# Kernel optimization log

Measured on AMD Instinct MI355X. Metric: run time of the kernel, lower is better.

## Reference

```python
import jax, jax.numpy as jnp
import numpy as np

NUM_TYPES = 8
IN_FEATURES = 1024
OUT_FEATURES = 1024
N = 65536


def setup_inputs() -> dict:
    key = jax.random.key(0)
    k_x, k_t, k_w, k_b = jax.random.split(key, 4)
    x = jax.random.normal(k_x, (N, IN_FEATURES), dtype=jnp.float32)
    types = jnp.sort(jax.random.randint(k_t, (N,), 0, NUM_TYPES, dtype=jnp.int32))
    # Per-type Linear params; PyTorch Linear stores weight as [out, in] and
    # computes x @ W.T + b. We store W as [T, in, out] (pre-transposed).
    bound = 1.0 / np.sqrt(IN_FEATURES)
    W = jax.random.uniform(k_w, (NUM_TYPES, IN_FEATURES, OUT_FEATURES), dtype=jnp.float32,
                           minval=-bound, maxval=bound)
    b = jax.random.uniform(k_b, (NUM_TYPES, OUT_FEATURES), dtype=jnp.float32,
                           minval=-bound, maxval=bound)
    return {"x": x, "types": types, "W": W, "b": b}


def reference(x, types, W, b):
    # out[n] = x[n] @ W[types[n]] + b[types[n]]
    # Small fixed loop over num_types: one masked GEMM per type (grouped GEMM).
    num_types = W.shape[0]
    out = jnp.zeros((x.shape[0], W.shape[2]), dtype=x.dtype)
    for t in range(num_types):
        mask = (types == t)[:, None]  # [N, 1]
        out = out + jnp.where(mask, x @ W[t] + b[t], 0.0)
    return out
```

## Files before the change

kernel.cpp:

```cpp
#include <hip/hip_runtime.h>
#include <hip/hip_bf16.h>

#define NROWS 65536
#define KDIM  1024
#define NOUT  1024
#define NTYPE 8

typedef __attribute__((ext_vector_type(8))) short bf16x8;
typedef __attribute__((ext_vector_type(4))) float f32x4;

__device__ __forceinline__ unsigned int pk2_rn(float a, float b) {
  unsigned int ua = __float_as_uint(a);
  unsigned int ub = __float_as_uint(b);
  ua += 0x7fffu + ((ua >> 16) & 1u);
  ub += 0x7fffu + ((ub >> 16) & 1u);
  return (ua >> 16) | (ub & 0xffff0000u);
}

__device__ __forceinline__ void async_cp16(const void* g, void* l) {
  __builtin_amdgcn_global_load_lds(
      (const __attribute__((address_space(1))) unsigned int*)g,
      (__attribute__((address_space(3))) unsigned int*)l, 16, 0, 0);
}

__global__ __launch_bounds__(256) void wtrans_kernel(
    const float* __restrict__ W, unsigned short* __restrict__ Wt) {
  __shared__ unsigned short T[64 * 66];
  unsigned int* Tw = (unsigned int*)T;

  const int ty = blockIdx.x;
  const int k0 = blockIdx.y * 64;
  const int n0 = blockIdx.z * 64;
  const float* src = W + (size_t)ty * (KDIM * NOUT);
  unsigned short* dst = Wt + (size_t)ty * (KDIM * NOUT);

  const int tid = threadIdx.x;
  const int k2 = tid >> 5;
  const int n2 = tid & 31;

#pragma unroll
  for (int p = 0; p < 4; ++p) {
    int kl = p * 16 + k2 * 2;
    float2 v0 = *(const float2*)(src + (size_t)(k0 + kl) * NOUT + n0 + n2 * 2);
    float2 v1 = *(const float2*)(src + (size_t)(k0 + kl + 1) * NOUT + n0 + n2 * 2);
    Tw[(n2 * 2) * 33 + p * 8 + k2]     = pk2_rn(v0.x, v1.x);
    Tw[(n2 * 2 + 1) * 33 + p * 8 + k2] = pk2_rn(v0.y, v1.y);
  }
  __syncthreads();

  const int c   = tid & 7;
  const int nl0 = tid >> 3;
#pragma unroll
  for (int p = 0; p < 2; ++p) {
    int nl = nl0 + p * 32;
    int ng = n0 + nl;
    const unsigned int* tw = Tw + nl * 33 + c * 4;
    uint4 o;
    o.x = tw[0]; o.y = tw[1]; o.z = tw[2]; o.w = tw[3];
    int kc = (k0 >> 3) + c;
    int G  = kc >> 2;
    int bp = (kc & 3) ^ ((ng >> 1) & 3);
    *(uint4*)(dst + (size_t)ng * KDIM + G * 32 + bp * 8) = o;
  }
}

__global__ __launch_bounds__(256) void typed_gemm_kernel(
    const float* __restrict__ x, const int* __restrict__ types,
    const unsigned short* __restrict__ Wt, const float* __restrict__ bias,
    float* __restrict__ out) {
  __shared__ unsigned short As[2][128 * 32];
  __shared__ unsigned short Bs[2][128 * 32];

  const int tid  = threadIdx.x;
  const int lane = tid & 63;
  const int wave = tid >> 6;
  const int quad = lane >> 4;
  const int l16  = lane & 15;

  const int wg   = blockIdx.y * gridDim.x + blockIdx.x;
  const int xcd  = wg & 7;
  const int idx  = wg >> 3;
  const int n0   = (idx & 7) * 128;
  const int m0   = ((xcd << 6) + (idx >> 3)) * 128;

  const int t0 = types[m0];
  const int t1 = types[m0 + 127];
  const bool multi = (t0 != t1);
  const int S = (t1 - t0 + 1) * 32;

  int stype[4], aoff[4];
  const float* agp[4];
#pragma unroll
  for (int r = 0; r < 4; ++r) {
    int idx2 = r * 256 + tid;
    int m = idx2 >> 3;
    int kc = idx2 & 7;
    stype[r] = types[m0 + m];
    int b  = kc >> 1;
    int h  = kc & 1;
    int bp = b ^ ((m >> 1) & 3);
    aoff[r] = m * 32 + bp * 8 + h * 4;
    agp[r]  = x + (size_t)(m0 + m) * KDIM + kc * 4;
  }

  const int mbase = (wave & 1) * 64;
  const int nbase = (wave >> 1) * 64;

  int ard[4], brd[4];
#pragma unroll
  for (int mt = 0; mt < 4; ++mt) {
    int m = mbase + mt * 16 + l16;
    ard[mt] = m * 32 + (quad ^ ((m >> 1) & 3)) * 8;
  }
#pragma unroll
  for (int nt = 0; nt < 4; ++nt) {
    int n = nbase + nt * 16 + l16;
    brd[nt] = n * 32 + (quad ^ ((n >> 1) & 3)) * 8;
  }

  f32x4 acc[4][4];
#pragma unroll
  for (int i = 0; i < 4; ++i)
#pragma unroll
    for (int j = 0; j < 4; ++j) acc[i][j] = (f32x4){0.f, 0.f, 0.f, 0.f};

  const int brow = lane >> 2;
  const int bchk = lane & 3;

  float4 av[4];

  auto stage_load = [&](int s, int buf) {
    const int t  = t0 + (s >> 5);
    const int kb = (s & 31) << 5;
#pragma unroll
    for (int r = 0; r < 4; ++r) av[r] = *(const float4*)(agp[r] + kb);
    const unsigned short* wbase = Wt + (size_t)t * (KDIM * NOUT);
    const int seg0 = wave * 2;
    const unsigned short* g0 =
        wbase + (size_t)(n0 + seg0 * 16 + brow) * KDIM + kb + bchk * 8;
    async_cp16(g0, &Bs[buf][seg0 * 512 + lane * 8]);
    async_cp16(g0 + (size_t)16 * KDIM, &Bs[buf][(seg0 + 1) * 512 + lane * 8]);
  };

  auto stage_write = [&](int s, int buf) {
    const int t = t0 + (s >> 5);
#pragma unroll
    for (int r = 0; r < 4; ++r) {
      uint2 p;
      p.x = pk2_rn(av[r].x, av[r].y);
      p.y = pk2_rn(av[r].z, av[r].w);
      if (stype[r] != t) { p.x = 0u; p.y = 0u; }
      *(uint2*)(&As[buf][aoff[r]]) = p;
    }
  };

  stage_load(0, 0);
  stage_write(0, 0);
  __syncthreads();

  for (int s = 0; s < S; ++s) {
    const int cur = s & 1;
    const int nxt = cur ^ 1;
    if (s + 1 < S) stage_load(s + 1, nxt);

    bf16x8 af[4], bfr[4];
#pragma unroll
    for (int i = 0; i < 4; ++i) af[i] = *(const bf16x8*)(&As[cur][ard[i]]);
#pragma unroll
    for (int i = 0; i < 4; ++i) bfr[i] = *(const bf16x8*)(&Bs[cur][brd[i]]);
#pragma unroll
    for (int mt = 0; mt < 4; ++mt)
#pragma unroll
      for (int nt = 0; nt < 4; ++nt)
        acc[mt][nt] = __builtin_amdgcn_mfma_f32_16x16x32_bf16(
            af[mt], bfr[nt], acc[mt][nt], 0, 0, 0);

    if (s + 1 < S) stage_write(s + 1, nxt);
    __syncthreads();
  }

  float bval[4];
  if (!multi) {
#pragma unroll
    for (int nt = 0; nt < 4; ++nt)
      bval[nt] = bias[t0 * NOUT + n0 + nbase + nt * 16 + l16];
  }
#pragma unroll
  for (int mt = 0; mt < 4; ++mt) {
#pragma unroll
    for (int reg = 0; reg < 4; ++reg) {
      int rl = mbase + mt * 16 + quad * 4 + reg;
      int grow = m0 + rl;
      float* orow = out + (size_t)grow * NOUT + n0 + nbase + l16;
      if (!multi) {
#pragma unroll
        for (int nt = 0; nt < 4; ++nt)
          orow[nt * 16] = acc[mt][nt][reg] + bval[nt];
      } else {
        int ty = types[grow];
#pragma unroll
        for (int nt = 0; nt < 4; ++nt)
          orow[nt * 16] =
              acc[mt][nt][reg] + bias[ty * NOUT + n0 + nbase + nt * 16 + l16];
      }
    }
  }
}

extern "C" void kernel_launch(void* const* d_in, const int* in_sizes, int n_in,
                              void* d_out, int out_size, void* d_ws,
                              size_t ws_size, hipStream_t stream) {
  const float* x     = (const float*)d_in[0];
  const int*   types = (const int*)d_in[1];
  const float* W     = (const float*)d_in[2];
  const float* b     = (const float*)d_in[3];
  float* out = (float*)d_out;
  unsigned short* Wt = (unsigned short*)d_ws;

  wtrans_kernel<<<dim3(NTYPE, KDIM / 64, NOUT / 64), 256, 0, stream>>>(W, Wt);
  typed_gemm_kernel<<<dim3(NOUT / 128, NROWS / 128), 256, 0, stream>>>(
      x, types, Wt, b, out);
}
```

Baseline: 751.7 us.

## Replace double-buffered K=32 pipeline with single-buffered K=64 stages

Drops the LDS double buffer and software pipelining in the typed GEMM main loop, and instead uses one buffer with a K tile of 64 per stage. This halves the number of stages and barriers. Each stage now loads, converts and stores A, issues async B copies, syncs, then runs two MFMA substeps. It removes the prefetch overlap, so global latency is exposed unless other resident blocks hide it.

```diff
diff --git a/kernel.cpp b/kernel.cpp
--- a/kernel.cpp
+++ b/kernel.cpp
@@ -68,8 +68,8 @@
     const float* __restrict__ x, const int* __restrict__ types,
     const unsigned short* __restrict__ Wt, const float* __restrict__ bias,
     float* __restrict__ out) {
-  __shared__ unsigned short As[2][128 * 32];
-  __shared__ unsigned short Bs[2][128 * 32];
+  __shared__ unsigned short As[128 * 64];
+  __shared__ unsigned short Bs[128 * 64];
 
   const int tid  = threadIdx.x;
   const int lane = tid & 63;
@@ -86,21 +86,22 @@
   const int t0 = types[m0];
   const int t1 = types[m0 + 127];
   const bool multi = (t0 != t1);
-  const int S = (t1 - t0 + 1) * 32;
-
-  int stype[4], aoff[4];
-  const float* agp[4];
-#pragma unroll
-  for (int r = 0; r < 4; ++r) {
+  const int S = (t1 - t0 + 1) * 16;
+
+  int stype[8], aoff[8], agof[8];
+#pragma unroll
+  for (int r = 0; r < 8; ++r) {
     int idx2 = r * 256 + tid;
-    int m = idx2 >> 3;
-    int kc = idx2 & 7;
+    int m  = idx2 >> 4;
+    int kc = idx2 & 15;
     stype[r] = types[m0 + m];
-    int b  = kc >> 1;
-    int h  = kc & 1;
+    int g  = kc >> 3;
+    int c  = kc & 7;
+    int b  = c >> 1;
+    int h  = c & 1;
     int bp = b ^ ((m >> 1) & 3);
-    aoff[r] = m * 32 + bp * 8 + h * 4;
-    agp[r]  = x + (size_t)(m0 + m) * KDIM + kc * 4;
+    aoff[r] = m * 64 + g * 32 + bp * 8 + h * 4;
+    agof[r] = (m0 + m) * KDIM + kc * 4;
   }
 
   const int mbase = (wave & 1) * 64;
@@ -110,12 +111,12 @@
 #pragma unroll
   for (int mt = 0; mt < 4; ++mt) {
     int m = mbase + mt * 16 + l16;
-    ard[mt] = m * 32 + (quad ^ ((m >> 1) & 3)) * 8;
+    ard[mt] = m * 64 + (quad ^ ((m >> 1) & 3)) * 8;
   }
 #pragma unroll
   for (int nt = 0; nt < 4; ++nt) {
     int n = nbase + nt * 16 + l16;
-    brd[nt] = n * 32 + (quad ^ ((n >> 1) & 3)) * 8;
+    brd[nt] = n * 64 + (quad ^ ((n >> 1) & 3)) * 8;
   }
 
   f32x4 acc[4][4];
@@ -124,58 +125,52 @@
 #pragma unroll
     for (int j = 0; j < 4; ++j) acc[i][j] = (f32x4){0.f, 0.f, 0.f, 0.f};
 
-  const int brow = lane >> 2;
-  const int bchk = lane & 3;
-
-  float4 av[4];
-
-  auto stage_load = [&](int s, int buf) {
-    const int t  = t0 + (s >> 5);
-    const int kb = (s & 31) << 5;
-#pragma unroll
-    for (int r = 0; r < 4; ++r) av[r] = *(const float4*)(agp[r] + kb);
-    const unsigned short* wbase = Wt + (size_t)t * (KDIM * NOUT);
-    const int seg0 = wave * 2;
-    const unsigned short* g0 =
-        wbase + (size_t)(n0 + seg0 * 16 + brow) * KDIM + kb + bchk * 8;
-    async_cp16(g0, &Bs[buf][seg0 * 512 + lane * 8]);
-    async_cp16(g0 + (size_t)16 * KDIM, &Bs[buf][(seg0 + 1) * 512 + lane * 8]);
-  };
-
-  auto stage_write = [&](int s, int buf) {
-    const int t = t0 + (s >> 5);
-#pragma unroll
-    for (int r = 0; r < 4; ++r) {
+  for (int s = 0; s < S; ++s) {
+    const int t  = t0 + (s >> 4);
+    const int kb = (s & 15) << 6;
+
+    float4 av[8];
+#pragma unroll
+    for (int r = 0; r < 8; ++r) av[r] = *(const float4*)(x + agof[r] + kb);
+
+    {
+      const unsigned short* wbase = Wt + (size_t)t * (KDIM * NOUT);
+#pragma unroll
+      for (int j = 0; j < 4; ++j) {
+        int grp = wave * 4 + j;
+        const unsigned short* g0 =
+            wbase + (size_t)(n0 + grp * 8 + (lane >> 3)) * KDIM + kb +
+            (lane & 7) * 8;
+        async_cp16(g0, &Bs[grp * 512 + lane * 8]);
+      }
+    }
+
+#pragma unroll
+    for (int r = 0; r < 8; ++r) {
       uint2 p;
       p.x = pk2_rn(av[r].x, av[r].y);
       p.y = pk2_rn(av[r].z, av[r].w);
       if (stype[r] != t) { p.x = 0u; p.y = 0u; }
-      *(uint2*)(&As[buf][aoff[r]]) = p;
-    }
-  };
-
-  stage_load(0, 0);
-  stage_write(0, 0);
-  __syncthreads();
-
-  for (int s = 0; s < S; ++s) {
-    const int cur = s & 1;
-    const int nxt = cur ^ 1;
-    if (s + 1 < S) stage_load(s + 1, nxt);
-
-    bf16x8 af[4], bfr[4];
-#pragma unroll
-    for (int i = 0; i < 4; ++i) af[i] = *(const bf16x8*)(&As[cur][ard[i]]);
-#pragma unroll
-    for (int i = 0; i < 4; ++i) bfr[i] = *(const bf16x8*)(&Bs[cur][brd[i]]);
-#pragma unroll
-    for (int mt = 0; mt < 4; ++mt)
-#pragma unroll
-      for (int nt = 0; nt < 4; ++nt)
-        acc[mt][nt] = __builtin_amdgcn_mfma_f32_16x16x32_bf16(
-            af[mt], bfr[nt], acc[mt][nt], 0, 0, 0);
-
-    if (s + 1 < S) stage_write(s + 1, nxt);
+      *(uint2*)(&As[aoff[r]]) = p;
+    }
+    __syncthreads();
+
+#pragma unroll
+    for (int kk = 0; kk < 2; ++kk) {
+      bf16x8 af[4], bfr[4];
+#pragma unroll
+      for (int i = 0; i < 4; ++i)
+        af[i] = *(const bf16x8*)(&As[ard[i] + kk * 32]);
+#pragma unroll
+      for (int i = 0; i < 4; ++i)
+        bfr[i] = *(const bf16x8*)(&Bs[brd[i] + kk * 32]);
+#pragma unroll
+      for (int mt = 0; mt < 4; ++mt)
+#pragma unroll
+        for (int nt = 0; nt < 4; ++nt)
+          acc[mt][nt] = __builtin_amdgcn_mfma_f32_16x16x32_bf16(
+              af[mt], bfr[nt], acc[mt][nt], 0, 0, 0);
+    }
     __syncthreads();
   }
 
```

Result: faster. 717.1 us (-4.6%).

## Replace double-buffered LDS pipeline with single-buffer synchronous loop per type

Applied to the files above, without the earlier changes.

Removes the double-buffered LDS staging and register prefetch of the next K-slice, replacing it with a nested loop over types and K. Each step loads the A and B tiles into a single LDS buffer, syncs, runs the MFMAs, then syncs again. This halves LDS use and cuts register pressure, which may raise occupancy. In exchange, global loads no longer overlap with MFMA work inside a block and there is an extra barrier per step.

```diff
diff --git a/kernel.cpp b/kernel.cpp
--- a/kernel.cpp
+++ b/kernel.cpp
@@ -68,8 +68,8 @@
     const float* __restrict__ x, const int* __restrict__ types,
     const unsigned short* __restrict__ Wt, const float* __restrict__ bias,
     float* __restrict__ out) {
-  __shared__ unsigned short As[2][128 * 32];
-  __shared__ unsigned short Bs[2][128 * 32];
+  __shared__ unsigned short As[128 * 32];
+  __shared__ unsigned short Bs[128 * 32];
 
   const int tid  = threadIdx.x;
   const int lane = tid & 63;
@@ -86,15 +86,15 @@
   const int t0 = types[m0];
   const int t1 = types[m0 + 127];
   const bool multi = (t0 != t1);
-  const int S = (t1 - t0 + 1) * 32;
-
-  int stype[4], aoff[4];
+
+  int srow[4], stype[4], aoff[4];
   const float* agp[4];
 #pragma unroll
   for (int r = 0; r < 4; ++r) {
     int idx2 = r * 256 + tid;
     int m = idx2 >> 3;
     int kc = idx2 & 7;
+    srow[r]  = m;
     stype[r] = types[m0 + m];
     int b  = kc >> 1;
     int h  = kc & 1;
@@ -127,56 +127,47 @@
   const int brow = lane >> 2;
   const int bchk = lane & 3;
 
-  float4 av[4];
-
-  auto stage_load = [&](int s, int buf) {
-    const int t  = t0 + (s >> 5);
-    const int kb = (s & 31) << 5;
-#pragma unroll
-    for (int r = 0; r < 4; ++r) av[r] = *(const float4*)(agp[r] + kb);
+  for (int t = t0; t <= t1; ++t) {
     const unsigned short* wbase = Wt + (size_t)t * (KDIM * NOUT);
-    const int seg0 = wave * 2;
-    const unsigned short* g0 =
-        wbase + (size_t)(n0 + seg0 * 16 + brow) * KDIM + kb + bchk * 8;
-    async_cp16(g0, &Bs[buf][seg0 * 512 + lane * 8]);
-    async_cp16(g0 + (size_t)16 * KDIM, &Bs[buf][(seg0 + 1) * 512 + lane * 8]);
-  };
-
-  auto stage_write = [&](int s, int buf) {
-    const int t = t0 + (s >> 5);
-#pragma unroll
-    for (int r = 0; r < 4; ++r) {
-      uint2 p;
-      p.x = pk2_rn(av[r].x, av[r].y);
-      p.y = pk2_rn(av[r].z, av[r].w);
-      if (stype[r] != t) { p.x = 0u; p.y = 0u; }
-      *(uint2*)(&As[buf][aoff[r]]) = p;
+    bool msk[4];
+#pragma unroll
+    for (int r = 0; r < 4; ++r) msk[r] = (stype[r] == t);
+
+    for (int kb = 0; kb < KDIM; kb += 32) {
+      {
+        int seg0 = wave * 2;
+        int seg1 = seg0 + 1;
+        const unsigned short* g0 =
+            wbase + (size_t)(n0 + seg0 * 16 + brow) * KDIM + kb + bchk * 8;
+        const unsigned short* g1 =
+            wbase + (size_t)(n0 + seg1 * 16 + brow) * KDIM + kb + bchk * 8;
+        async_cp16(g0, &Bs[seg0 * 512 + lane * 8]);
+        async_cp16(g1, &Bs[seg1 * 512 + lane * 8]);
+      }
+#pragma unroll
+      for (int r = 0; r < 4; ++r) {
+        float4 v = *(const float4*)(agp[r] + kb);
+        uint2 p;
+        p.x = pk2_rn(v.x, v.y);
+        p.y = pk2_rn(v.z, v.w);
+        if (!msk[r]) { p.x = 0u; p.y = 0u; }
+        *(uint2*)(&As[aoff[r]]) = p;
+      }
+      __syncthreads();
+
+      bf16x8 af[4], bfr[4];
+#pragma unroll
+      for (int i = 0; i < 4; ++i) af[i] = *(const bf16x8*)(&As[ard[i]]);
+#pragma unroll
+      for (int i = 0; i < 4; ++i) bfr[i] = *(const bf16x8*)(&Bs[brd[i]]);
+#pragma unroll
+      for (int mt = 0; mt < 4; ++mt)
+#pragma unroll
+        for (int nt = 0; nt < 4; ++nt)
+          acc[mt][nt] = __builtin_amdgcn_mfma_f32_16x16x32_bf16(
+              af[mt], bfr[nt], acc[mt][nt], 0, 0, 0);
+      __syncthreads();
     }
-  };
-
-  stage_load(0, 0);
-  stage_write(0, 0);
-  __syncthreads();
-
-  for (int s = 0; s < S; ++s) {
-    const int cur = s & 1;
-    const int nxt = cur ^ 1;
-    if (s + 1 < S) stage_load(s + 1, nxt);
-
-    bf16x8 af[4], bfr[4];
-#pragma unroll
-    for (int i = 0; i < 4; ++i) af[i] = *(const bf16x8*)(&As[cur][ard[i]]);
-#pragma unroll
-    for (int i = 0; i < 4; ++i) bfr[i] = *(const bf16x8*)(&Bs[cur][brd[i]]);
-#pragma unroll
-    for (int mt = 0; mt < 4; ++mt)
-#pragma unroll
-      for (int nt = 0; nt < 4; ++nt)
-        acc[mt][nt] = __builtin_amdgcn_mfma_f32_16x16x32_bf16(
-            af[mt], bfr[nt], acc[mt][nt], 0, 0, 0);
-
-    if (s + 1 < S) stage_write(s + 1, nxt);
-    __syncthreads();
   }
 
   float bval[4];
```

After: 687.4 us. 1.09x faster.
